# Performance work log

Measured on AMD Instinct MI355X. Metric: run time of the kernel, lower is better.

Reference implementation:

```python
import jax, jax.numpy as jnp
import numpy as np

EPS = 1e-5
GROUPS = 8

def group_norm(x, gamma, beta):
    b, c, h, w = x.shape
    xg = x.reshape(b, GROUPS, c // GROUPS, h, w)
    mean = xg.mean(axis=(2, 3, 4), keepdims=True)
    var = xg.var(axis=(2, 3, 4), keepdims=True)
    xn = ((xg - mean) * jax.lax.rsqrt(var + EPS)).reshape(b, c, h, w)
    return xn * gamma[None, :, None, None] + beta[None, :, None, None]

def conv1x1(x, w, b):
    # x: (B,C,H,W), w: (Cout,Cin), b: (Cout,)
    return jnp.einsum('bchw,oc->bohw', x, w) + b[None, :, None, None]

def setup_inputs() -> dict:
    key = jax.random.key(0)
    ks = jax.random.split(key, 10)
    C = 512
    x = jax.random.normal(ks[0], (4, C, 64, 64), dtype=jnp.float32)
    s = 1.0 / np.sqrt(C)
    inp = {
        'x': x,
        'gamma': jnp.ones((C,), jnp.float32),
        'beta': jnp.zeros((C,), jnp.float32),
        'wq': jax.random.uniform(ks[1], (C, C), jnp.float32, -s, s),
        'bq': jax.random.uniform(ks[2], (C,), jnp.float32, -s, s),
        'wk': jax.random.uniform(ks[3], (C, C), jnp.float32, -s, s),
        'bk': jax.random.uniform(ks[4], (C,), jnp.float32, -s, s),
        'wv': jax.random.uniform(ks[5], (C, C), jnp.float32, -s, s),
        'bv': jax.random.uniform(ks[6], (C,), jnp.float32, -s, s),
        'wo': jax.random.uniform(ks[7], (C, C), jnp.float32, -s, s),
        'bo': jax.random.uniform(ks[8], (C,), jnp.float32, -s, s),
    }
    return inp

def reference(x, gamma, beta, wq, bq, wk, bk, wv, bv, wo, bo):
    b, c, hd, wd = x.shape
    h = group_norm(x, gamma, beta)
    q = conv1x1(h, wq, bq).reshape(b, c, hd * wd).transpose(0, 2, 1)  # (b, hw, c)
    k = conv1x1(h, wk, bk).reshape(b, c, hd * wd)                      # (b, c, hw)
    v = conv1x1(h, wv, bv).reshape(b, c, hd * wd).transpose(0, 2, 1)  # (b, hw, c)
    attn = jnp.einsum('bqc,bck->bqk', q, k) * (c ** -0.5)
    attn = jax.nn.softmax(attn, axis=2)
    out = jnp.einsum('bqk,bkc->bqc', attn, v)                          # (b, hw, c)
    out = out.transpose(0, 2, 1).reshape(b, c, hd, wd)
    out = conv1x1(out, wo, bo)
    return x + out
```

## Files before the change

### kernel.cpp

```cpp
#include <hip/hip_runtime.h>
#include <stdint.h>

#define B_ 4
#define C_ 512
#define S_ 4096
#define G_ 8
#define CPG_ 64
#define EPS_ 1e-5f
#define SCALE_ 0.04419417382415922f
#define DTHR_ 4.0f

typedef _Float16 f16;
typedef _Float16 f16x8 __attribute__((ext_vector_type(8)));
typedef _Float16 f16x4 __attribute__((ext_vector_type(4)));
typedef unsigned short u16x8 __attribute__((ext_vector_type(8)));
typedef unsigned short u16x4 __attribute__((ext_vector_type(4)));
typedef unsigned int u32x4 __attribute__((ext_vector_type(4)));
typedef float f32x4 __attribute__((ext_vector_type(4)));

__device__ __forceinline__ float bf2f(unsigned short u) {
    union { unsigned int i; float f; } v; v.i = ((unsigned int)u) << 16; return v.f;
}
__device__ __forceinline__ unsigned short f2bf(float f) {
    union { float f; unsigned int i; } v; v.f = f;
    unsigned int i = v.i;
    return (unsigned short)((i + 0x7fffu + ((i >> 16) & 1u)) >> 16);
}
__device__ __forceinline__ unsigned char f2e4m3(float f) {
    return (unsigned char)(__builtin_amdgcn_cvt_pk_fp8_f32(f, f, 0, false) & 0xff);
}

__device__ __forceinline__ void bar_lgkm() {
    asm volatile("s_waitcnt lgkmcnt(0)" ::: "memory");
    __builtin_amdgcn_s_barrier();
}

#define DPPF(x, ctrl) __int_as_float(__builtin_amdgcn_update_dpp(0, __float_as_int(x), ctrl, 0xf, 0xf, true))
#define DPP_MAX16(x) do { \
    x = fmaxf(x, DPPF(x, 0x121)); \
    x = fmaxf(x, DPPF(x, 0x122)); \
    x = fmaxf(x, DPPF(x, 0x124)); \
    x = fmaxf(x, DPPF(x, 0x128)); \
} while (0)
#define DPP_SUM16(x) do { \
    x += DPPF(x, 0x121); \
    x += DPPF(x, 0x122); \
    x += DPPF(x, 0x124); \
    x += DPPF(x, 0x128); \
} while (0)

__global__ void detect_kernel(const void* __restrict__ gamma, int* __restrict__ flag, float* __restrict__ stats) {
    *flag = (((const unsigned int*)gamma)[0] != 0x3F800000u) ? 1 : 0;
    for (int i = 0; i < 64; ++i) stats[i] = 0.f;
}

__global__ __launch_bounds__(256) void cvt_weights(const void* __restrict__ w0, const void* __restrict__ w1,
                                                   const void* __restrict__ w2, const void* __restrict__ w3,
                                                   f16* __restrict__ dst, const int* __restrict__ flagp) {
    const void* srcs[4] = {w0, w1, w2, w3};
    const void* s = srcs[blockIdx.y];
    f16* d = dst + (size_t)blockIdx.y * (C_ * C_);
    int i4 = blockIdx.x * 256 + threadIdx.x;
    f16x4 o;
    if (*flagp) {
        u16x4 u = ((const u16x4*)s)[i4];
#pragma unroll
        for (int j = 0; j < 4; ++j) o[j] = (f16)bf2f(u[j]);
    } else {
        f32x4 u = ((const f32x4*)s)[i4];
#pragma unroll
        for (int j = 0; j < 4; ++j) o[j] = (f16)u[j];
    }
    ((f16x4*)d)[i4] = o;
}

__global__ __launch_bounds__(512) void cvt_vecs(const void* __restrict__ g, const void* __restrict__ be,
                                                const void* __restrict__ b1, const void* __restrict__ b2,
                                                const void* __restrict__ b3, const void* __restrict__ b4,
                                                float* __restrict__ dst, const int* __restrict__ flagp) {
    const void* srcs[6] = {g, be, b1, b2, b3, b4};
    const void* s = srcs[blockIdx.x];
    int i = threadIdx.x;
    dst[blockIdx.x * 512 + i] = (*flagp) ? bf2f(((const unsigned short*)s)[i]) : ((const float*)s)[i];
}

__global__ __launch_bounds__(1024) void gn_stats(const void* __restrict__ xraw, const int* __restrict__ flagp,
                                                 float* __restrict__ stats) {
    int bg = blockIdx.x >> 3, ch = blockIdx.x & 7;
    const int PER = CPG_ * S_ / 8;
    float s = 0.f, ss = 0.f;
    if (*flagp) {
        const u16x8* p = (const u16x8*)((const unsigned short*)xraw + (size_t)bg * CPG_ * S_ + (size_t)ch * PER);
        for (int i = threadIdx.x; i < PER / 8; i += 1024) {
            u16x8 u = p[i];
#pragma unroll
            for (int j = 0; j < 8; ++j) { float f = bf2f(u[j]); s += f; ss += f * f; }
        }
    } else {
        const f32x4* p = (const f32x4*)((const float*)xraw + (size_t)bg * CPG_ * S_ + (size_t)ch * PER);
        for (int i = threadIdx.x; i < PER / 4; i += 1024) {
            f32x4 u = p[i];
#pragma unroll
            for (int j = 0; j < 4; ++j) { float f = u[j]; s += f; ss += f * f; }
        }
    }
    __shared__ float rs[1024], rss[1024];
    rs[threadIdx.x] = s; rss[threadIdx.x] = ss;
    __syncthreads();
    for (int st = 512; st > 0; st >>= 1) {
        if (threadIdx.x < st) { rs[threadIdx.x] += rs[threadIdx.x + st]; rss[threadIdx.x] += rss[threadIdx.x + st]; }
        __syncthreads();
    }
    if (threadIdx.x == 0) {
        atomicAdd(&stats[bg * 2], rs[0]);
        atomicAdd(&stats[bg * 2 + 1], rss[0]);
    }
}

__global__ __launch_bounds__(256) void gn_apply_t(const void* __restrict__ xraw, const int* __restrict__ flagp,
                                                  const float* __restrict__ gammaF, const float* __restrict__ betaF,
                                                  const float* __restrict__ stats, f16* __restrict__ hT) {
    int s0 = blockIdx.x * 32, c0 = blockIdx.y * 32, b = blockIdx.z;
    __shared__ float tile[32][33];
    int t = threadIdx.x;
    int cr = t >> 3, ct = t & 7;
    int c = c0 + cr;
    int g = c >> 6;
    const float Ninv = 1.f / (float)(CPG_ * S_);
    float mean = stats[(b * G_ + g) * 2] * Ninv;
    float var = stats[(b * G_ + g) * 2 + 1] * Ninv - mean * mean;
    float rstd = rsqrtf(var + EPS_);
    float ga = gammaF[c], be = betaF[c];
    size_t xi = ((size_t)(b * C_ + c)) * S_ + s0;
    float v[4];
    if (*flagp) {
        u16x4 u = *(const u16x4*)((const unsigned short*)xraw + xi + ct * 4);
#pragma unroll
        for (int j = 0; j < 4; ++j) v[j] = bf2f(u[j]);
    } else {
        f32x4 u = *(const f32x4*)((const float*)xraw + xi + ct * 4);
#pragma unroll
        for (int j = 0; j < 4; ++j) v[j] = u[j];
    }
#pragma unroll
    for (int j = 0; j < 4; ++j)
        tile[cr][ct * 4 + j] = (v[j] - mean) * rstd * ga + be;
    __syncthreads();
    int sr = t >> 3, cv = t & 7;
    f16x4 o;
#pragma unroll
    for (int j = 0; j < 4; ++j) o[j] = (f16)tile[cv * 4 + j][sr];
    *(f16x4*)(hT + ((size_t)b * S_ + s0 + sr) * C_ + c0 + cv * 4) = o;
}

__global__ __launch_bounds__(256) void gemm_qk8(const f16* __restrict__ A, const f16* __restrict__ W,
                                                const float* __restrict__ biasF, unsigned char* __restrict__ out8) {
    int b = blockIdx.y;
    int s0 = (blockIdx.x >> 3) * 64;
    int o0 = (blockIdx.x & 7) * 64;
    __shared__ __attribute__((aligned(16))) f16 As[64][40];
    __shared__ __attribute__((aligned(16))) f16 Bs[64][40];
    int t = threadIdx.x;
    int w = t >> 6, lane = t & 63, l15 = lane & 15, quad = lane >> 4;
    f32x4 acc[4] = {};
    const f16* Ag = A + ((size_t)b * S_ + s0) * C_;
    int row = t >> 2, cp = (t & 3) * 8;
    const f16* aSrc = Ag + (size_t)row * C_ + cp;
    const f16* bSrc = W + (size_t)(o0 + row) * C_ + cp;
    f16x8 paA = *(const f16x8*)(aSrc);
    f16x8 pbA = *(const f16x8*)(bSrc);
    f16x8 paB = *(const f16x8*)(aSrc + 32);
    f16x8 pbB = *(const f16x8*)(bSrc + 32);
#pragma unroll
    for (int kk = 0; kk < 16; kk += 2) {
        *(f16x8*)(&As[row][cp]) = paA;
        *(f16x8*)(&Bs[row][cp]) = pbA;
        bar_lgkm();
        int ka = (kk * 32 + 64) & 511;
        paA = *(const f16x8*)(aSrc + ka);
        pbA = *(const f16x8*)(bSrc + ka);
        {
            f16x8 a = *(const f16x8*)&As[w * 16 + l15][quad * 8];
#pragma unroll
            for (int nt = 0; nt < 4; ++nt) {
                f16x8 bb = *(const f16x8*)&Bs[nt * 16 + l15][quad * 8];
                acc[nt] = __builtin_amdgcn_mfma_f32_16x16x32_f16(a, bb, acc[nt], 0, 0, 0);
            }
        }
        bar_lgkm();
        *(f16x8*)(&As[row][cp]) = paB;
        *(f16x8*)(&Bs[row][cp]) = pbB;
        bar_lgkm();
        int kb = (kk * 32 + 96) & 511;
        paB = *(const f16x8*)(aSrc + kb);
        pbB = *(const f16x8*)(bSrc + kb);
        {
            f16x8 a = *(const f16x8*)&As[w * 16 + l15][quad * 8];
#pragma unroll
            for (int nt = 0; nt < 4; ++nt) {
                f16x8 bb = *(const f16x8*)&Bs[nt * 16 + l15][quad * 8];
                acc[nt] = __builtin_amdgcn_mfma_f32_16x16x32_f16(a, bb, acc[nt], 0, 0, 0);
            }
        }
        bar_lgkm();
    }
#pragma unroll
    for (int nt = 0; nt < 4; ++nt) {
        int o = o0 + nt * 16 + l15;
        float bv = biasF[o];
#pragma unroll
        for (int r = 0; r < 4; ++r) {
            int s = s0 + w * 16 + quad * 4 + r;
            out8[((size_t)b * S_ + s) * C_ + o] = f2e4m3(acc[nt][r] + bv);
        }
    }
}

__global__ __launch_bounds__(256) void gemm_vt8(const f16* __restrict__ hT, const f16* __restrict__ W,
                                                const float* __restrict__ biasF, unsigned char* __restrict__ v8) {
    int b = blockIdx.y;
    int o0 = (blockIdx.x >> 6) * 64;
    int s0 = (blockIdx.x & 63) * 64;
    __shared__ __attribute__((aligned(16))) f16 As[64][40];
    __shared__ __attribute__((aligned(16))) f16 Bs[64][40];
    int t = threadIdx.x;
    int w = t >> 6, lane = t & 63, l15 = lane & 15, quad = lane >> 4;
    f32x4 acc[4] = {};
    const f16* Bg = hT + ((size_t)b * S_ + s0) * C_;
    int row = t >> 2, cp = (t & 3) * 8;
    const f16* aSrc = W + (size_t)(o0 + row) * C_ + cp;
    const f16* bSrc = Bg + (size_t)row * C_ + cp;
    f16x8 paA = *(const f16x8*)(aSrc);
    f16x8 pbA = *(const f16x8*)(bSrc);
    f16x8 paB = *(const f16x8*)(aSrc + 32);
    f16x8 pbB = *(const f16x8*)(bSrc + 32);
#pragma unroll
    for (int kk = 0; kk < 16; kk += 2) {
        *(f16x8*)(&As[row][cp]) = paA;
        *(f16x8*)(&Bs[row][cp]) = pbA;
        bar_lgkm();
        int ka = (kk * 32 + 64) & 511;
        paA = *(const f16x8*)(aSrc + ka);
        pbA = *(const f16x8*)(bSrc + ka);
        {
            f16x8 a = *(const f16x8*)&As[w * 16 + l15][quad * 8];
#pragma unroll
            for (int nt = 0; nt < 4; ++nt) {
                f16x8 bb = *(const f16x8*)&Bs[nt * 16 + l15][quad * 8];
                acc[nt] = __builtin_amdgcn_mfma_f32_16x16x32_f16(a, bb, acc[nt], 0, 0, 0);
            }
        }
        bar_lgkm();
        *(f16x8*)(&As[row][cp]) = paB;
        *(f16x8*)(&Bs[row][cp]) = pbB;
        bar_lgkm();
        int kb = (kk * 32 + 96) & 511;
        paB = *(const f16x8*)(aSrc + kb);
        pbB = *(const f16x8*)(bSrc + kb);
        {
            f16x8 a = *(const f16x8*)&As[w * 16 + l15][quad * 8];
#pragma unroll
            for (int nt = 0; nt < 4; ++nt) {
                f16x8 bb = *(const f16x8*)&Bs[nt * 16 + l15][quad * 8];
                acc[nt] = __builtin_amdgcn_mfma_f32_16x16x32_f16(a, bb, acc[nt], 0, 0, 0);
            }
        }
        bar_lgkm();
    }
    size_t tb = ((size_t)b * 64 + (s0 >> 6)) * 512;
#pragma unroll
    for (int nt = 0; nt < 4; ++nt) {
#pragma unroll
        for (int r = 0; r < 4; ++r) {
            int o = o0 + w * 16 + quad * 4 + r;
            v8[(tb + o) * 64 + nt * 16 + l15] = f2e4m3(acc[nt][r] + biasF[o]);
        }
    }
}

#define KST 136
#define VST 72
#define SLOT 9216
#define QST 528
#define RING_OFF 67584
#define PL_OFF   104448
#define REDM_OFF 113664
#define REDL_OFF 114688
#define SMEM_TOTAL 115712

__global__ __launch_bounds__(1024, 4) void flash_attn(const unsigned char* __restrict__ Q8,
                                                      const unsigned char* __restrict__ K8,
                                                      const unsigned char* __restrict__ V8,
                                                      f16* __restrict__ Op0, f16* __restrict__ Op1,
                                                      float* __restrict__ Ml, float* __restrict__ Ll) {
    extern __shared__ unsigned char smem[];
    unsigned char* Qlds = smem;
    unsigned char* ring = smem + RING_OFF;
    unsigned char* Pl   = smem + PL_OFF;
    float* redm = (float*)(smem + REDM_OFF);
    float* redl = (float*)(smem + REDL_OFF);

    const int id = blockIdx.x;
    const int b = (id & 7) >> 1;
    const int ks = id & 1;
    const int q0 = (id >> 3) * 128;
    const int kbase = ks * (S_ / 2);
    const int NT = (S_ / 2) / 64;

    const int t = threadIdx.x;
    const int w = t >> 6, lane = t & 63, l15 = lane & 15, quad = lane >> 4;
    const int qw = w >> 1;
    const int cw = w & 1;
    const int qrow = qw * 16 + l15;

    const unsigned char* Kb = K8 + (size_t)b * S_ * C_;
    const unsigned char* Vb = V8 + (size_t)b * 64 * 512 * 64;

    const int kwo = (((t & 15) >> 3) * SLOT) + ((t >> 4) * KST) + ((t & 7) * 16);
    const unsigned char* ksrc0 = Kb + (((size_t)(kbase + (t >> 4))) << 9) + ((t & 15) << 4);
    const int row16 = t >> 2;
    const int sel = (row16 >> 6) & 1;
    const int vr = (row16 & 63) + ((row16 >> 7) << 6);
    const int vwo = sel * SLOT + vr * VST + (t & 3) * 16;
    const int c0 = (row16 < 128) ? row16 : (128 + row16);
    const unsigned char* vsrc0 = Vb + (((size_t)(kbase >> 6)) << 15) + (c0 << 6) + ((t & 3) << 4);

    {
        const unsigned char* Qb = Q8 + ((size_t)b * S_ + q0) * C_;
        int qr = t >> 5, g16 = t & 31;
#pragma unroll
        for (int sg = 0; sg < 4; ++sg) {
            u32x4 v = *(const u32x4*)(Qb + (size_t)(sg * 32 + qr) * C_ + g16 * 16);
            *(u32x4*)&Qlds[(sg * 32 + qr) * QST + g16 * 16] = v;
        }
    }

    f32x4 accO[16] = {};
    float mrow[4], lrow[4];
#pragma unroll
    for (int r = 0; r < 4; ++r) { mrow[r] = -1e30f; lrow[r] = 0.f; }

    u32x4 pr0 = *(const u32x4*)(ksrc0);
    u32x4 pr1 = *(const u32x4*)(ksrc0 + 256);

    for (int tile = 0; tile < NT; ++tile) {
        const size_t toff = (size_t)tile << 15;
        const size_t tnoff = (size_t)((tile + 1) & 31) << 15;
        f32x4 accS[2] = {};

        {
            *(u32x4*)(ring + kwo) = pr0;
            pr0 = *(const u32x4*)(vsrc0 + toff);
            bar_lgkm();
            __builtin_amdgcn_s_setprio(1);
#pragma unroll
            for (int half = 0; half < 2; ++half) {
                const unsigned char* buf = &ring[half * SLOT];
#pragma unroll
                for (int cc2 = 0; cc2 < 4; ++cc2) {
                    long a = *(const long*)&Qlds[qrow * QST + (half * 4 + cc2) * 32 + quad * 8];
#pragma unroll
                    for (int nt = 0; nt < 2; ++nt) {
                        int row = cw * 32 + nt * 16 + l15;
                        long bb = *(const long*)&buf[row * KST + (cc2 * 4 + quad) * 8];
                        accS[nt] = __builtin_amdgcn_mfma_f32_16x16x32_fp8_fp8(a, bb, accS[nt], 0, 0, 0);
                    }
                }
            }
            __builtin_amdgcn_s_setprio(0);
        }
        {
            *(u32x4*)(ring + 2 * SLOT + kwo) = pr1;
            pr1 = *(const u32x4*)(vsrc0 + toff + 8192);
            bar_lgkm();
            __builtin_amdgcn_s_setprio(1);
#pragma unroll
            for (int half = 0; half < 2; ++half) {
                const unsigned char* buf = &ring[(2 + half) * SLOT];
#pragma unroll
                for (int cc2 = 0; cc2 < 4; ++cc2) {
                    long a = *(const long*)&Qlds[qrow * QST + ((2 + half) * 4 + cc2) * 32 + quad * 8];
#pragma unroll
                    for (int nt = 0; nt < 2; ++nt) {
                        int row = cw * 32 + nt * 16 + l15;
                        long bb = *(const long*)&buf[row * KST + (cc2 * 4 + quad) * 8];
                        accS[nt] = __builtin_amdgcn_mfma_f32_16x16x32_fp8_fp8(a, bb, accS[nt], 0, 0, 0);
                    }
                }
            }
            __builtin_amdgcn_s_setprio(0);
        }

        float sc[2][4];
#pragma unroll
        for (int nt = 0; nt < 2; ++nt)
#pragma unroll
            for (int r = 0; r < 4; ++r) sc[nt][r] = accS[nt][r] * SCALE_;

        float mx[4];
#pragma unroll
        for (int r = 0; r < 4; ++r) {
            mx[r] = fmaxf(sc[0][r], sc[1][r]);
            DPP_MAX16(mx[r]);
        }
        if (l15 == 0) {
#pragma unroll
            for (int r = 0; r < 4; ++r) redm[cw * 128 + qw * 16 + quad * 4 + r] = mx[r];
        }
        bar_lgkm();
        float alpha[4];
        int need = 0;
#pragma unroll
        for (int r = 0; r < 4; ++r) {
            int rowq = qw * 16 + quad * 4 + r;
            float mnew = fmaxf(mrow[r], fmaxf(redm[rowq], redm[128 + rowq]));
            if (mnew - mrow[r] > DTHR_) {
                alpha[r] = __expf(mrow[r] - mnew);
                mrow[r] = mnew;
                need = 1;
            } else {
                alpha[r] = 1.f;
            }
        }
        float p[2][4], psum[4];
#pragma unroll
        for (int r = 0; r < 4; ++r) {
            p[0][r] = __expf(sc[0][r] - mrow[r]);
            p[1][r] = __expf(sc[1][r] - mrow[r]);
            psum[r] = p[0][r] + p[1][r];
            DPP_SUM16(psum[r]);
        }
        if (l15 == 0) {
#pragma unroll
            for (int r = 0; r < 4; ++r) redl[cw * 128 + qw * 16 + quad * 4 + r] = psum[r];
        }
#pragma unroll
        for (int nt = 0; nt < 2; ++nt)
#pragma unroll
            for (int r = 0; r < 4; ++r)
                Pl[(qw * 16 + quad * 4 + r) * VST + cw * 32 + nt * 16 + l15] = f2e4m3(p[nt][r]);

        {
            *(u32x4*)(ring + vwo) = pr0;
            pr0 = *(const u32x4*)(ksrc0 + tnoff);
            bar_lgkm();
#pragma unroll
            for (int r = 0; r < 4; ++r) {
                int rowq = qw * 16 + quad * 4 + r;
                lrow[r] = lrow[r] * alpha[r] + redl[rowq] + redl[128 + rowq];
            }
            if (__any(need)) {
#pragma unroll
                for (int nt = 0; nt < 16; ++nt)
#pragma unroll
                    for (int r = 0; r < 4; ++r) accO[nt][r] *= alpha[r];
            }
            __builtin_amdgcn_s_setprio(1);
#pragma unroll
            for (int half = 0; half < 2; ++half) {
                const unsigned char* buf = &ring[half * SLOT];
#pragma unroll
                for (int st = 0; st < 2; ++st) {
                    long a = *(const long*)&Pl[(qw * 16 + l15) * VST + st * 32 + quad * 8];
#pragma unroll
                    for (int nt = 0; nt < 4; ++nt) {
                        int vrow = cw * 64 + nt * 16 + l15;
                        long bb = *(const long*)&buf[vrow * VST + (st * 4 + quad) * 8];
                        accO[half * 4 + nt] = __builtin_amdgcn_mfma_f32_16x16x32_fp8_fp8(a, bb, accO[half * 4 + nt], 0, 0, 0);
                    }
                }
            }
            __builtin_amdgcn_s_setprio(0);
        }
        {
            *(u32x4*)(ring + 2 * SLOT + vwo) = pr1;
            pr1 = *(const u32x4*)(ksrc0 + tnoff + 256);
            bar_lgkm();
            __builtin_amdgcn_s_setprio(1);
#pragma unroll
            for (int half = 0; half < 2; ++half) {
                const unsigned char* buf = &ring[(2 + half) * SLOT];
#pragma unroll
                for (int st = 0; st < 2; ++st) {
                    long a = *(const long*)&Pl[(qw * 16 + l15) * VST + st * 32 + quad * 8];
#pragma unroll
                    for (int nt = 0; nt < 4; ++nt) {
                        int vrow = cw * 64 + nt * 16 + l15;
                        long bb = *(const long*)&buf[vrow * VST + (st * 4 + quad) * 8];
                        accO[(2 + half) * 4 + nt] = __builtin_amdgcn_mfma_f32_16x16x32_fp8_fp8(a, bb, accO[(2 + half) * 4 + nt], 0, 0, 0);
                    }
                }
            }
            __builtin_amdgcn_s_setprio(0);
        }
    }

    __syncthreads();
    float li[4];
#pragma unroll
    for (int r = 0; r < 4; ++r) li[r] = 1.f / lrow[r];
    f16* Ob = (ks ? Op1 : Op0) + ((size_t)b * S_ + q0) * C_;
    f16* elds = (f16*)smem;
#pragma unroll
    for (int p = 0; p < 8; ++p) {
        if (qw == p) {
#pragma unroll
            for (int ntg = 0; ntg < 16; ++ntg) {
                int cc = cw * 256 + (ntg >> 2) * 64 + (ntg & 3) * 16 + l15;
#pragma unroll
                for (int r = 0; r < 4; ++r)
                    elds[(quad * 4 + r) * 520 + cc] = (f16)(accO[ntg][r] * li[r]);
            }
        }
        __syncthreads();
        {
            int erow = t >> 6, g8 = t & 63;
            f16x8 v = *(const f16x8*)&elds[erow * 520 + g8 * 8];
            *(f16x8*)(Ob + (size_t)(p * 16 + erow) * C_ + g8 * 8) = v;
        }
        __syncthreads();
    }
    if (cw == 0 && l15 == 0) {
        size_t base = (size_t)(b * 2 + ks) * S_ + q0 + qw * 16 + quad * 4;
#pragma unroll
        for (int r = 0; r < 4; ++r) { Ml[base + r] = mrow[r]; Ll[base + r] = lrow[r]; }
    }
}

__global__ __launch_bounds__(256) void merge_halves(const f16* __restrict__ Op0, const f16* __restrict__ Op1,
                                                    const float* __restrict__ Ml, const float* __restrict__ Ll,
                                                    f16* __restrict__ O) {
    int idx = blockIdx.x * 256 + threadIdx.x;
    int row = idx >> 6;
    int c8 = (idx & 63) * 8;
    int b = row >> 12, q = row & 4095;
    size_t i1 = (size_t)(b * 2) * S_ + q;
    size_t i2 = (size_t)(b * 2 + 1) * S_ + q;
    float m1 = Ml[i1], m2 = Ml[i2], l1 = Ll[i1], l2 = Ll[i2];
    float m = fmaxf(m1, m2);
    float u1 = __expf(m1 - m) * l1, u2 = __expf(m2 - m) * l2;
    float inv = 1.f / (u1 + u2);
    u1 *= inv; u2 *= inv;
    size_t ro = (size_t)(b * 4096 + q) * C_ + c8;
    f16x8 o1 = *(const f16x8*)(Op0 + ro);
    f16x8 o2 = *(const f16x8*)(Op1 + ro);
    f16x8 o;
#pragma unroll
    for (int j = 0; j < 8; ++j) o[j] = (f16)(u1 * (float)o1[j] + u2 * (float)o2[j]);
    *(f16x8*)(O + ro) = o;
}

__global__ __launch_bounds__(256) void gemm_out(const f16* __restrict__ A, const f16* __restrict__ W,
                                                const float* __restrict__ biasF,
                                                const void* __restrict__ xraw, const int* __restrict__ flagp,
                                                void* __restrict__ outraw) {
    int b = blockIdx.y;
    int s0 = (blockIdx.x >> 3) * 64;
    int o0 = (blockIdx.x & 7) * 64;
    __shared__ __attribute__((aligned(16))) f16 As[64][40];
    __shared__ __attribute__((aligned(16))) f16 Bs[64][40];
    int t = threadIdx.x;
    int w = t >> 6, lane = t & 63, l15 = lane & 15, quad = lane >> 4;
    f32x4 acc[4] = {};
    const f16* Ag = A + ((size_t)b * S_ + s0) * C_;
    int row = t >> 2, cp = (t & 3) * 8;
    const f16* aSrc = Ag + (size_t)row * C_ + cp;
    const f16* bSrc = W + (size_t)(o0 + row) * C_ + cp;
    f16x8 paA = *(const f16x8*)(aSrc);
    f16x8 pbA = *(const f16x8*)(bSrc);
    f16x8 paB = *(const f16x8*)(aSrc + 32);
    f16x8 pbB = *(const f16x8*)(bSrc + 32);
#pragma unroll
    for (int kk = 0; kk < 16; kk += 2) {
        *(f16x8*)(&As[row][cp]) = paA;
        *(f16x8*)(&Bs[row][cp]) = pbA;
        bar_lgkm();
        int ka = (kk * 32 + 64) & 511;
        paA = *(const f16x8*)(aSrc + ka);
        pbA = *(const f16x8*)(bSrc + ka);
        {
            f16x8 a = *(const f16x8*)&As[w * 16 + l15][quad * 8];
#pragma unroll
            for (int nt = 0; nt < 4; ++nt) {
                f16x8 bb = *(const f16x8*)&Bs[nt * 16 + l15][quad * 8];
                acc[nt] = __builtin_amdgcn_mfma_f32_16x16x32_f16(a, bb, acc[nt], 0, 0, 0);
            }
        }
        bar_lgkm();
        *(f16x8*)(&As[row][cp]) = paB;
        *(f16x8*)(&Bs[row][cp]) = pbB;
        bar_lgkm();
        int kb = (kk * 32 + 96) & 511;
        paB = *(const f16x8*)(aSrc + kb);
        pbB = *(const f16x8*)(bSrc + kb);
        {
            f16x8 a = *(const f16x8*)&As[w * 16 + l15][quad * 8];
#pragma unroll
            for (int nt = 0; nt < 4; ++nt) {
                f16x8 bb = *(const f16x8*)&Bs[nt * 16 + l15][quad * 8];
                acc[nt] = __builtin_amdgcn_mfma_f32_16x16x32_f16(a, bb, acc[nt], 0, 0, 0);
            }
        }
        bar_lgkm();
    }
    int flg = *flagp;
#pragma unroll
    for (int nt = 0; nt < 4; ++nt) {
        int o = o0 + nt * 16 + l15;
        float bv = biasF[o];
        int sbase = s0 + w * 16 + quad * 4;
        size_t xi = ((size_t)b * C_ + o) * S_ + sbase;
        if (flg) {
            u16x4 xr = *(const u16x4*)((const unsigned short*)xraw + xi);
            u16x4 res;
#pragma unroll
            for (int r = 0; r < 4; ++r) res[r] = f2bf(acc[nt][r] + bv + bf2f(xr[r]));
            *(u16x4*)((unsigned short*)outraw + xi) = res;
        } else {
            f32x4 xr = *(const f32x4*)((const float*)xraw + xi);
            f32x4 res;
#pragma unroll
            for (int r = 0; r < 4; ++r) res[r] = acc[nt][r] + bv + xr[r];
            *(f32x4*)((float*)outraw + xi) = res;
        }
    }
}

extern "C" void kernel_launch(void* const* d_in, const int* in_sizes, int n_in,
                              void* d_out, int out_size, void* d_ws, size_t ws_size,
                              hipStream_t stream) {
    const void* x     = d_in[0];
    const void* gamma = d_in[1];
    const void* beta  = d_in[2];
    const void* wq    = d_in[3];
    const void* bq    = d_in[4];
    const void* wk    = d_in[5];
    const void* bk    = d_in[6];
    const void* wv    = d_in[7];
    const void* bv    = d_in[8];
    const void* wo    = d_in[9];
    const void* bo    = d_in[10];

    char* ws = (char*)d_ws;
    size_t off = 0;
    int* flag = (int*)(ws + off); off += 256;
    float* stats = (float*)(ws + off); off += 512;
    float* vecF = (float*)(ws + off); off += 6 * 512 * 4;
    float* Ml = (float*)(ws + off); off += (size_t)2 * B_ * S_ * 4;
    float* Ll = (float*)(ws + off); off += (size_t)2 * B_ * S_ * 4;
    f16* w16 = (f16*)(ws + off); off += (size_t)4 * C_ * C_ * 2;
    const size_t TEN = (size_t)B_ * S_ * C_ * 2;
    const size_t TE8 = (size_t)B_ * S_ * C_;
    f16* hT  = (f16*)(ws + off); off += TEN;
    unsigned char* q8 = (unsigned char*)(ws + off); off += TE8;
    unsigned char* k8 = (unsigned char*)(ws + off); off += TE8;
    unsigned char* v8 = (unsigned char*)(ws + off); off += TE8;
    f16* o_  = (f16*)(ws + off); off += TEN;
    f16* op1 = (f16*)(ws + off); off += TEN;
    if (ws_size < off) return;

    float* gammaF = vecF + 0 * 512;
    float* betaF  = vecF + 1 * 512;
    float* bqF    = vecF + 2 * 512;
    float* bkF    = vecF + 3 * 512;
    float* bvF    = vecF + 4 * 512;
    float* boF    = vecF + 5 * 512;
    f16* wq16 = w16 + 0 * (size_t)C_ * C_;
    f16* wk16 = w16 + 1 * (size_t)C_ * C_;
    f16* wv16 = w16 + 2 * (size_t)C_ * C_;
    f16* wo16 = w16 + 3 * (size_t)C_ * C_;

    hipFuncSetAttribute((const void*)flash_attn, hipFuncAttributeMaxDynamicSharedMemorySize, SMEM_TOTAL);

    detect_kernel<<<dim3(1), dim3(1), 0, stream>>>(gamma, flag, stats);
    cvt_weights<<<dim3(256, 4), dim3(256), 0, stream>>>(wq, wk, wv, wo, w16, flag);
    cvt_vecs<<<dim3(6), dim3(512), 0, stream>>>(gamma, beta, bq, bk, bv, bo, vecF, flag);
    gn_stats<<<dim3(256), dim3(1024), 0, stream>>>(x, flag, stats);
    gn_apply_t<<<dim3(128, 16, 4), dim3(256), 0, stream>>>(x, flag, gammaF, betaF, stats, hT);
    gemm_qk8<<<dim3(512, 4), dim3(256), 0, stream>>>(hT, wq16, bqF, q8);
    gemm_qk8<<<dim3(512, 4), dim3(256), 0, stream>>>(hT, wk16, bkF, k8);
    gemm_vt8<<<dim3(512, 4), dim3(256), 0, stream>>>(hT, wv16, bvF, v8);
    flash_attn<<<dim3(256), dim3(1024), SMEM_TOTAL, stream>>>(q8, k8, v8, hT, op1, Ml, Ll);
    merge_halves<<<dim3((B_ * S_ * C_ / 8) / 256), dim3(256), 0, stream>>>(hT, op1, Ml, Ll, o_);
    gemm_out<<<dim3(512, 4), dim3(256), 0, stream>>>(o_, wo16, boF, x, flag, d_out);
}
```

Before: 409.4 us.

## Halve flash-attn query tile to 64 rows, fold softmax scale into Q

The flash attention kernel now uses 512-thread blocks covering 64 query rows instead of 1024 threads covering 128, with twice as many blocks and a smaller LDS footprint. The K/V prefetch is redone so each thread loads two 16-byte chunks per stage. The softmax scale and log2(e) are folded into the Q projection before FP8 quantization, and the exponentials switch to native exp2. The rescale threshold rises to 5.5. Smaller tiles raise occupancy but double K/V reloads per query. Pre-scaling Q changes the FP8 quantization range, and the higher threshold lets partial sums grow larger before rescaling.

```diff
diff --git a/kernel.cpp b/kernel.cpp
--- a/kernel.cpp
+++ b/kernel.cpp
@@ -8,7 +8,8 @@
 #define CPG_ 64
 #define EPS_ 1e-5f
 #define SCALE_ 0.04419417382415922f
-#define DTHR_ 4.0f
+#define LOG2E_ 1.4426950408889634f
+#define DTHR_ 5.5f
 
 typedef _Float16 f16;
 typedef _Float16 f16x8 __attribute__((ext_vector_type(8)));
@@ -28,6 +29,9 @@
 }
 __device__ __forceinline__ unsigned char f2e4m3(float f) {
     return (unsigned char)(__builtin_amdgcn_cvt_pk_fp8_f32(f, f, 0, false) & 0xff);
+}
+__device__ __forceinline__ float fast_exp2(float x) {
+    return __builtin_amdgcn_exp2f(x);
 }
 
 __device__ __forceinline__ void bar_lgkm() {
@@ -154,7 +158,8 @@
 }
 
 __global__ __launch_bounds__(256) void gemm_qk8(const f16* __restrict__ A, const f16* __restrict__ W,
-                                                const float* __restrict__ biasF, unsigned char* __restrict__ out8) {
+                                                const float* __restrict__ biasF, unsigned char* __restrict__ out8,
+                                                float ascale) {
     int b = blockIdx.y;
     int s0 = (blockIdx.x >> 3) * 64;
     int o0 = (blockIdx.x & 7) * 64;
@@ -211,7 +216,7 @@
 #pragma unroll
         for (int r = 0; r < 4; ++r) {
             int s = s0 + w * 16 + quad * 4 + r;
-            out8[((size_t)b * S_ + s) * C_ + o] = f2e4m3(acc[nt][r] + bv);
+            out8[((size_t)b * S_ + s) * C_ + o] = f2e4m3((acc[nt][r] + bv) * ascale);
         }
     }
 }
@@ -282,28 +287,28 @@
 #define VST 72
 #define SLOT 9216
 #define QST 528
-#define RING_OFF 67584
-#define PL_OFF   104448
-#define REDM_OFF 113664
-#define REDL_OFF 114688
-#define SMEM_TOTAL 115712
-
-__global__ __launch_bounds__(1024, 4) void flash_attn(const unsigned char* __restrict__ Q8,
-                                                      const unsigned char* __restrict__ K8,
-                                                      const unsigned char* __restrict__ V8,
-                                                      f16* __restrict__ Op0, f16* __restrict__ Op1,
-                                                      float* __restrict__ Ml, float* __restrict__ Ll) {
+#define PL_OFF   36864
+#define REDM_OFF 41472
+#define REDL_OFF 41984
+#define Q_OFF    42496
+#define SMEM_TOTAL 76288
+
+__global__ __launch_bounds__(512, 4) void flash_attn(const unsigned char* __restrict__ Q8,
+                                                     const unsigned char* __restrict__ K8,
+                                                     const unsigned char* __restrict__ V8,
+                                                     f16* __restrict__ Op0, f16* __restrict__ Op1,
+                                                     float* __restrict__ Ml, float* __restrict__ Ll) {
     extern __shared__ unsigned char smem[];
-    unsigned char* Qlds = smem;
-    unsigned char* ring = smem + RING_OFF;
+    unsigned char* ring = smem;
     unsigned char* Pl   = smem + PL_OFF;
     float* redm = (float*)(smem + REDM_OFF);
     float* redl = (float*)(smem + REDL_OFF);
+    unsigned char* Qlds = smem + Q_OFF;
 
     const int id = blockIdx.x;
     const int b = (id & 7) >> 1;
     const int ks = id & 1;
-    const int q0 = (id >> 3) * 128;
+    const int q0 = (id >> 3) * 64;
     const int kbase = ks * (S_ / 2);
     const int NT = (S_ / 2) / 64;
 
@@ -317,21 +322,22 @@
     const unsigned char* Vb = V8 + (size_t)b * 64 * 512 * 64;
 
     const int kwo = (((t & 15) >> 3) * SLOT) + ((t >> 4) * KST) + ((t & 7) * 16);
-    const unsigned char* ksrc0 = Kb + (((size_t)(kbase + (t >> 4))) << 9) + ((t & 15) << 4);
+    const unsigned char* ksrc = Kb + (((size_t)(kbase + (t >> 4))) << 9) + ((t & 15) << 4);
     const int row16 = t >> 2;
-    const int sel = (row16 >> 6) & 1;
-    const int vr = (row16 & 63) + ((row16 >> 7) << 6);
-    const int vwo = sel * SLOT + vr * VST + (t & 3) * 16;
-    const int c0 = (row16 < 128) ? row16 : (128 + row16);
-    const unsigned char* vsrc0 = Vb + (((size_t)(kbase >> 6)) << 15) + (c0 << 6) + ((t & 3) << 4);
+    const int vwo = ((row16 >> 6) & 1) * SLOT + (row16 & 63) * VST + (t & 3) * 16;
+    const unsigned char* vsrc = Vb + (((size_t)(kbase >> 6)) << 15) + (row16 << 6) + ((t & 3) << 4);
+
+    u32x4 prA = *(const u32x4*)(ksrc);
+    u32x4 prB = *(const u32x4*)(ksrc + 16384);
 
     {
         const unsigned char* Qb = Q8 + ((size_t)b * S_ + q0) * C_;
         int qr = t >> 5, g16 = t & 31;
 #pragma unroll
-        for (int sg = 0; sg < 4; ++sg) {
-            u32x4 v = *(const u32x4*)(Qb + (size_t)(sg * 32 + qr) * C_ + g16 * 16);
-            *(u32x4*)&Qlds[(sg * 32 + qr) * QST + g16 * 16] = v;
+        for (int j = 0; j < 4; ++j) {
+            int row = j * 16 + qr;
+            u32x4 v = *(const u32x4*)(Qb + (size_t)row * C_ + g16 * 16);
+            *(u32x4*)&Qlds[row * QST + g16 * 16] = v;
         }
     }
 
@@ -339,9 +345,6 @@
     float mrow[4], lrow[4];
 #pragma unroll
     for (int r = 0; r < 4; ++r) { mrow[r] = -1e30f; lrow[r] = 0.f; }
-
-    u32x4 pr0 = *(const u32x4*)(ksrc0);
-    u32x4 pr1 = *(const u32x4*)(ksrc0 + 256);
 
     for (int tile = 0; tile < NT; ++tile) {
         const size_t toff = (size_t)tile << 15;
@@ -349,8 +352,10 @@
         f32x4 accS[2] = {};
 
         {
-            *(u32x4*)(ring + kwo) = pr0;
-            pr0 = *(const u32x4*)(vsrc0 + toff);
+            *(u32x4*)(ring + kwo) = prA;
+            *(u32x4*)(ring + kwo + 32 * KST) = prB;
+            prA = *(const u32x4*)(ksrc + toff + 256);
+            prB = *(const u32x4*)(ksrc + toff + 256 + 16384);
             bar_lgkm();
             __builtin_amdgcn_s_setprio(1);
 #pragma unroll
@@ -370,8 +375,10 @@
             __builtin_amdgcn_s_setprio(0);
         }
         {
-            *(u32x4*)(ring + 2 * SLOT + kwo) = pr1;
-            pr1 = *(const u32x4*)(vsrc0 + toff + 8192);
+            *(u32x4*)(ring + 2 * SLOT + kwo) = prA;
+            *(u32x4*)(ring + 2 * SLOT + kwo + 32 * KST) = prB;
+            prA = *(const u32x4*)(vsrc + toff);
+            prB = *(const u32x4*)(vsrc + toff + 16384);
             bar_lgkm();
             __builtin_amdgcn_s_setprio(1);
 #pragma unroll
@@ -391,21 +398,15 @@
             __builtin_amdgcn_s_setprio(0);
         }
 
-        float sc[2][4];
-#pragma unroll
-        for (int nt = 0; nt < 2; ++nt)
-#pragma unroll
-            for (int r = 0; r < 4; ++r) sc[nt][r] = accS[nt][r] * SCALE_;
-
         float mx[4];
 #pragma unroll
         for (int r = 0; r < 4; ++r) {
-            mx[r] = fmaxf(sc[0][r], sc[1][r]);
+            mx[r] = fmaxf(accS[0][r], accS[1][r]);
             DPP_MAX16(mx[r]);
         }
         if (l15 == 0) {
 #pragma unroll
-            for (int r = 0; r < 4; ++r) redm[cw * 128 + qw * 16 + quad * 4 + r] = mx[r];
+            for (int r = 0; r < 4; ++r) redm[cw * 64 + qw * 16 + quad * 4 + r] = mx[r];
         }
         bar_lgkm();
         float alpha[4];
@@ -413,9 +414,9 @@
 #pragma unroll
         for (int r = 0; r < 4; ++r) {
             int rowq = qw * 16 + quad * 4 + r;
-            float mnew = fmaxf(mrow[r], fmaxf(redm[rowq], redm[128 + rowq]));
+            float mnew = fmaxf(mrow[r], fmaxf(redm[rowq], redm[64 + rowq]));
             if (mnew - mrow[r] > DTHR_) {
-                alpha[r] = __expf(mrow[r] - mnew);
+                alpha[r] = fast_exp2(mrow[r] - mnew);
                 mrow[r] = mnew;
                 need = 1;
             } else {
@@ -425,14 +426,14 @@
         float p[2][4], psum[4];
 #pragma unroll
         for (int r = 0; r < 4; ++r) {
-            p[0][r] = __expf(sc[0][r] - mrow[r]);
-            p[1][r] = __expf(sc[1][r] - mrow[r]);
+            p[0][r] = fast_exp2(accS[0][r] - mrow[r]);
+            p[1][r] = fast_exp2(accS[1][r] - mrow[r]);
             psum[r] = p[0][r] + p[1][r];
             DPP_SUM16(psum[r]);
         }
         if (l15 == 0) {
 #pragma unroll
-            for (int r = 0; r < 4; ++r) redl[cw * 128 + qw * 16 + quad * 4 + r] = psum[r];
+            for (int r = 0; r < 4; ++r) redl[cw * 64 + qw * 16 + quad * 4 + r] = psum[r];
         }
 #pragma unroll
         for (int nt = 0; nt < 2; ++nt)
@@ -441,13 +442,15 @@
                 Pl[(qw * 16 + quad * 4 + r) * VST + cw * 32 + nt * 16 + l15] = f2e4m3(p[nt][r]);
 
         {
-            *(u32x4*)(ring + vwo) = pr0;
-            pr0 = *(const u32x4*)(ksrc0 + tnoff);
+            *(u32x4*)(ring + vwo) = prA;
+            *(u32x4*)(ring + vwo + 64 * VST) = prB;
+            prA = *(const u32x4*)(vsrc + toff + 8192);
+            prB = *(const u32x4*)(vsrc + toff + 8192 + 16384);
             bar_lgkm();
 #pragma unroll
             for (int r = 0; r < 4; ++r) {
                 int rowq = qw * 16 + quad * 4 + r;
-                lrow[r] = lrow[r] * alpha[r] + redl[rowq] + redl[128 + rowq];
+                lrow[r] = lrow[r] * alpha[r] + redl[rowq] + redl[64 + rowq];
             }
             if (__any(need)) {
 #pragma unroll
@@ -473,8 +476,10 @@
             __builtin_amdgcn_s_setprio(0);
         }
         {
-            *(u32x4*)(ring + 2 * SLOT + vwo) = pr1;
-            pr1 = *(const u32x4*)(ksrc0 + tnoff + 256);
+            *(u32x4*)(ring + 2 * SLOT + vwo) = prA;
+            *(u32x4*)(ring + 2 * SLOT + vwo + 64 * VST) = prB;
+            prA = *(const u32x4*)(ksrc + tnoff);
+            prB = *(const u32x4*)(ksrc + tnoff + 16384);
             bar_lgkm();
             __builtin_amdgcn_s_setprio(1);
 #pragma unroll
@@ -502,7 +507,7 @@
     f16* Ob = (ks ? Op1 : Op0) + ((size_t)b * S_ + q0) * C_;
     f16* elds = (f16*)smem;
 #pragma unroll
-    for (int p = 0; p < 8; ++p) {
+    for (int p = 0; p < 4; ++p) {
         if (qw == p) {
 #pragma unroll
             for (int ntg = 0; ntg < 16; ++ntg) {
@@ -513,8 +518,10 @@
             }
         }
         __syncthreads();
-        {
-            int erow = t >> 6, g8 = t & 63;
+#pragma unroll
+        for (int e = 0; e < 2; ++e) {
+            int erow = (t >> 6) + e * 8;
+            int g8 = t & 63;
             f16x8 v = *(const f16x8*)&elds[erow * 520 + g8 * 8];
             *(f16x8*)(Ob + (size_t)(p * 16 + erow) * C_ + g8 * 8) = v;
         }
@@ -538,7 +545,7 @@
     size_t i2 = (size_t)(b * 2 + 1) * S_ + q;
     float m1 = Ml[i1], m2 = Ml[i2], l1 = Ll[i1], l2 = Ll[i2];
     float m = fmaxf(m1, m2);
-    float u1 = __expf(m1 - m) * l1, u2 = __expf(m2 - m) * l2;
+    float u1 = fast_exp2(m1 - m) * l1, u2 = fast_exp2(m2 - m) * l2;
     float inv = 1.f / (u1 + u2);
     u1 *= inv; u2 *= inv;
     size_t ro = (size_t)(b * 4096 + q) * C_ + c8;
@@ -670,17 +677,17 @@
     f16* wv16 = w16 + 2 * (size_t)C_ * C_;
     f16* wo16 = w16 + 3 * (size_t)C_ * C_;
 
-    hipFuncSetAttribute((const void*)flash_attn, hipFuncAttributeMaxDynamicSharedMemorySize, SMEM_TOTAL);
+    (void)hipFuncSetAttribute((const void*)flash_attn, hipFuncAttributeMaxDynamicSharedMemorySize, SMEM_TOTAL);
 
     detect_kernel<<<dim3(1), dim3(1), 0, stream>>>(gamma, flag, stats);
     cvt_weights<<<dim3(256, 4), dim3(256), 0, stream>>>(wq, wk, wv, wo, w16, flag);
     cvt_vecs<<<dim3(6), dim3(512), 0, stream>>>(gamma, beta, bq, bk, bv, bo, vecF, flag);
     gn_stats<<<dim3(256), dim3(1024), 0, stream>>>(x, flag, stats);
     gn_apply_t<<<dim3(128, 16, 4), dim3(256), 0, stream>>>(x, flag, gammaF, betaF, stats, hT);
-    gemm_qk8<<<dim3(512, 4), dim3(256), 0, stream>>>(hT, wq16, bqF, q8);
-    gemm_qk8<<<dim3(512, 4), dim3(256), 0, stream>>>(hT, wk16, bkF, k8);
+    gemm_qk8<<<dim3(512, 4), dim3(256), 0, stream>>>(hT, wq16, bqF, q8, SCALE_ * LOG2E_);
+    gemm_qk8<<<dim3(512, 4), dim3(256), 0, stream>>>(hT, wk16, bkF, k8, 1.0f);
     gemm_vt8<<<dim3(512, 4), dim3(256), 0, stream>>>(hT, wv16, bvF, v8);
-    flash_attn<<<dim3(256), dim3(1024), SMEM_TOTAL, stream>>>(q8, k8, v8, hT, op1, Ml, Ll);
+    flash_attn<<<dim3(512), dim3(512), SMEM_TOTAL, stream>>>(q8, k8, v8, hT, op1, Ml, Ll);
     merge_halves<<<dim3((B_ * S_ * C_ / 8) / 256), dim3(256), 0, stream>>>(hT, op1, Ml, Ll, o_);
     gemm_out<<<dim3(512, 4), dim3(256), 0, stream>>>(o_, wo16, boF, x, flag, d_out);
 }
```

Result: slower. 444.1 us (+8.5%).

## Use 128x128 GEMM tiles and fold softmax scale and log2e into Q

Applied to the files above, without the earlier changes.

Replaces the three 64x64-tile projection GEMMs with a shared 128x128-tile core in which each wave computes a 4x4 block of MFMA tiles. This raises data reuse per shared-memory load and cuts block count. The softmax scale times log2(e) is folded into the Q projection before fp8 quantisation, so the attention kernel drops its per-score multiply and uses hardware exp2. The rescale threshold is also raised. Scaling Q before the fp8 cast changes quantisation error, and a larger threshold allows larger unnormalised exponents.

```diff
diff --git a/kernel.cpp b/kernel.cpp
--- a/kernel.cpp
+++ b/kernel.cpp
@@ -8,7 +8,8 @@
 #define CPG_ 64
 #define EPS_ 1e-5f
 #define SCALE_ 0.04419417382415922f
-#define DTHR_ 4.0f
+#define LOG2E_ 1.4426950408889634f
+#define DTHR_ 5.5f
 
 typedef _Float16 f16;
 typedef _Float16 f16x8 __attribute__((ext_vector_type(8)));
@@ -28,6 +29,9 @@
 }
 __device__ __forceinline__ unsigned char f2e4m3(float f) {
     return (unsigned char)(__builtin_amdgcn_cvt_pk_fp8_f32(f, f, 0, false) & 0xff);
+}
+__device__ __forceinline__ float fast_exp2(float x) {
+    return __builtin_amdgcn_exp2f(x);
 }
 
 __device__ __forceinline__ void bar_lgkm() {
@@ -153,127 +157,117 @@
     *(f16x4*)(hT + ((size_t)b * S_ + s0 + sr) * C_ + c0 + cv * 4) = o;
 }
 
+#define GEMM128_CORE(Aptr, Bptr)                                                             \
+    __shared__ __attribute__((aligned(16))) f16 As[128][40];                                  \
+    __shared__ __attribute__((aligned(16))) f16 Bs[128][40];                                  \
+    int t = threadIdx.x;                                                                      \
+    int w = t >> 6, lane = t & 63, l15 = lane & 15, quad = lane >> 4;                         \
+    int wr = w >> 1, wc = w & 1;                                                              \
+    f32x4 acc[4][4] = {};                                                                     \
+    int srow = t >> 1, scol = (t & 1) * 8;                                                    \
+    const f16* aS = (Aptr) + (size_t)srow * C_ + scol;                                        \
+    const f16* bS = (Bptr) + (size_t)srow * C_ + scol;                                        \
+    f16x8 pa0 = *(const f16x8*)(aS);                                                          \
+    f16x8 pa1 = *(const f16x8*)(aS + 16);                                                     \
+    f16x8 pb0 = *(const f16x8*)(bS);                                                          \
+    f16x8 pb1 = *(const f16x8*)(bS + 16);                                                     \
+    _Pragma("unroll")                                                                         \
+    for (int kk = 0; kk < 16; ++kk) {                                                         \
+        *(f16x8*)(&As[srow][scol]) = pa0;                                                     \
+        *(f16x8*)(&As[srow][scol + 16]) = pa1;                                                \
+        *(f16x8*)(&Bs[srow][scol]) = pb0;                                                     \
+        *(f16x8*)(&Bs[srow][scol + 16]) = pb1;                                                \
+        int kn = ((kk + 1) & 15) * 32;                                                        \
+        pa0 = *(const f16x8*)(aS + kn);                                                       \
+        pa1 = *(const f16x8*)(aS + kn + 16);                                                  \
+        pb0 = *(const f16x8*)(bS + kn);                                                       \
+        pb1 = *(const f16x8*)(bS + kn + 16);                                                  \
+        bar_lgkm();                                                                           \
+        f16x8 af[4], bf[4];                                                                   \
+        _Pragma("unroll")                                                                     \
+        for (int i = 0; i < 4; ++i) {                                                         \
+            af[i] = *(const f16x8*)&As[wr * 64 + i * 16 + l15][quad * 8];                     \
+            bf[i] = *(const f16x8*)&Bs[wc * 64 + i * 16 + l15][quad * 8];                     \
+        }                                                                                     \
+        _Pragma("unroll")                                                                     \
+        for (int mi = 0; mi < 4; ++mi)                                                        \
+            _Pragma("unroll")                                                                 \
+            for (int ni = 0; ni < 4; ++ni)                                                    \
+                acc[mi][ni] = __builtin_amdgcn_mfma_f32_16x16x32_f16(af[mi], bf[ni], acc[mi][ni], 0, 0, 0); \
+        bar_lgkm();                                                                           \
+    }
+
 __global__ __launch_bounds__(256) void gemm_qk8(const f16* __restrict__ A, const f16* __restrict__ W,
-                                                const float* __restrict__ biasF, unsigned char* __restrict__ out8) {
-    int b = blockIdx.y;
-    int s0 = (blockIdx.x >> 3) * 64;
-    int o0 = (blockIdx.x & 7) * 64;
-    __shared__ __attribute__((aligned(16))) f16 As[64][40];
-    __shared__ __attribute__((aligned(16))) f16 Bs[64][40];
-    int t = threadIdx.x;
-    int w = t >> 6, lane = t & 63, l15 = lane & 15, quad = lane >> 4;
-    f32x4 acc[4] = {};
-    const f16* Ag = A + ((size_t)b * S_ + s0) * C_;
-    int row = t >> 2, cp = (t & 3) * 8;
-    const f16* aSrc = Ag + (size_t)row * C_ + cp;
-    const f16* bSrc = W + (size_t)(o0 + row) * C_ + cp;
-    f16x8 paA = *(const f16x8*)(aSrc);
-    f16x8 pbA = *(const f16x8*)(bSrc);
-    f16x8 paB = *(const f16x8*)(aSrc + 32);
-    f16x8 pbB = *(const f16x8*)(bSrc + 32);
-#pragma unroll
-    for (int kk = 0; kk < 16; kk += 2) {
-        *(f16x8*)(&As[row][cp]) = paA;
-        *(f16x8*)(&Bs[row][cp]) = pbA;
-        bar_lgkm();
-        int ka = (kk * 32 + 64) & 511;
-        paA = *(const f16x8*)(aSrc + ka);
-        pbA = *(const f16x8*)(bSrc + ka);
-        {
-            f16x8 a = *(const f16x8*)&As[w * 16 + l15][quad * 8];
-#pragma unroll
-            for (int nt = 0; nt < 4; ++nt) {
-                f16x8 bb = *(const f16x8*)&Bs[nt * 16 + l15][quad * 8];
-                acc[nt] = __builtin_amdgcn_mfma_f32_16x16x32_f16(a, bb, acc[nt], 0, 0, 0);
-            }
-        }
-        bar_lgkm();
-        *(f16x8*)(&As[row][cp]) = paB;
-        *(f16x8*)(&Bs[row][cp]) = pbB;
-        bar_lgkm();
-        int kb = (kk * 32 + 96) & 511;
-        paB = *(const f16x8*)(aSrc + kb);
-        pbB = *(const f16x8*)(bSrc + kb);
-        {
-            f16x8 a = *(const f16x8*)&As[w * 16 + l15][quad * 8];
-#pragma unroll
-            for (int nt = 0; nt < 4; ++nt) {
-                f16x8 bb = *(const f16x8*)&Bs[nt * 16 + l15][quad * 8];
-                acc[nt] = __builtin_amdgcn_mfma_f32_16x16x32_f16(a, bb, acc[nt], 0, 0, 0);
-            }
-        }
-        bar_lgkm();
-    }
-#pragma unroll
-    for (int nt = 0; nt < 4; ++nt) {
-        int o = o0 + nt * 16 + l15;
-        float bv = biasF[o];
-#pragma unroll
-        for (int r = 0; r < 4; ++r) {
-            int s = s0 + w * 16 + quad * 4 + r;
-            out8[((size_t)b * S_ + s) * C_ + o] = f2e4m3(acc[nt][r] + bv);
+                                                const float* __restrict__ biasF, unsigned char* __restrict__ out8,
+                                                float ascale) {
+    int m0 = (blockIdx.x >> 2) * 128;
+    int n0 = (blockIdx.x & 3) * 128;
+    GEMM128_CORE(A + (size_t)m0 * C_, W + (size_t)n0 * C_)
+#pragma unroll
+    for (int ni = 0; ni < 4; ++ni) {
+        int n = n0 + wc * 64 + ni * 16 + l15;
+        float bv = biasF[n];
+#pragma unroll
+        for (int mi = 0; mi < 4; ++mi) {
+            int mb = m0 + wr * 64 + mi * 16 + quad * 4;
+#pragma unroll
+            for (int r = 0; r < 4; ++r)
+                out8[(size_t)(mb + r) * C_ + n] = f2e4m3((acc[mi][ni][r] + bv) * ascale);
         }
     }
 }
 
 __global__ __launch_bounds__(256) void gemm_vt8(const f16* __restrict__ hT, const f16* __restrict__ W,
                                                 const float* __restrict__ biasF, unsigned char* __restrict__ v8) {
-    int b = blockIdx.y;
-    int o0 = (blockIdx.x >> 6) * 64;
-    int s0 = (blockIdx.x & 63) * 64;
-    __shared__ __attribute__((aligned(16))) f16 As[64][40];
-    __shared__ __attribute__((aligned(16))) f16 Bs[64][40];
-    int t = threadIdx.x;
-    int w = t >> 6, lane = t & 63, l15 = lane & 15, quad = lane >> 4;
-    f32x4 acc[4] = {};
-    const f16* Bg = hT + ((size_t)b * S_ + s0) * C_;
-    int row = t >> 2, cp = (t & 3) * 8;
-    const f16* aSrc = W + (size_t)(o0 + row) * C_ + cp;
-    const f16* bSrc = Bg + (size_t)row * C_ + cp;
-    f16x8 paA = *(const f16x8*)(aSrc);
-    f16x8 pbA = *(const f16x8*)(bSrc);
-    f16x8 paB = *(const f16x8*)(aSrc + 32);
-    f16x8 pbB = *(const f16x8*)(bSrc + 32);
-#pragma unroll
-    for (int kk = 0; kk < 16; kk += 2) {
-        *(f16x8*)(&As[row][cp]) = paA;
-        *(f16x8*)(&Bs[row][cp]) = pbA;
-        bar_lgkm();
-        int ka = (kk * 32 + 64) & 511;
-        paA = *(const f16x8*)(aSrc + ka);
-        pbA = *(const f16x8*)(bSrc + ka);
-        {
-            f16x8 a = *(const f16x8*)&As[w * 16 + l15][quad * 8];
-#pragma unroll
-            for (int nt = 0; nt < 4; ++nt) {
-                f16x8 bb = *(const f16x8*)&Bs[nt * 16 + l15][quad * 8];
-                acc[nt] = __builtin_amdgcn_mfma_f32_16x16x32_f16(a, bb, acc[nt], 0, 0, 0);
-            }
-        }
-        bar_lgkm();
-        *(f16x8*)(&As[row][cp]) = paB;
-        *(f16x8*)(&Bs[row][cp]) = pbB;
-        bar_lgkm();
-        int kb = (kk * 32 + 96) & 511;
-        paB = *(const f16x8*)(aSrc + kb);
-        pbB = *(const f16x8*)(bSrc + kb);
-        {
-            f16x8 a = *(const f16x8*)&As[w * 16 + l15][quad * 8];
-#pragma unroll
-            for (int nt = 0; nt < 4; ++nt) {
-                f16x8 bb = *(const f16x8*)&Bs[nt * 16 + l15][quad * 8];
-                acc[nt] = __builtin_amdgcn_mfma_f32_16x16x32_f16(a, bb, acc[nt], 0, 0, 0);
-            }
-        }
-        bar_lgkm();
-    }
-    size_t tb = ((size_t)b * 64 + (s0 >> 6)) * 512;
-#pragma unroll
-    for (int nt = 0; nt < 4; ++nt) {
-#pragma unroll
-        for (int r = 0; r < 4; ++r) {
-            int o = o0 + w * 16 + quad * 4 + r;
-            v8[(tb + o) * 64 + nt * 16 + l15] = f2e4m3(acc[nt][r] + biasF[o]);
+    int m0 = (blockIdx.x & 3) * 128;
+    int n0 = (blockIdx.x >> 2) * 128;
+    GEMM128_CORE(W + (size_t)m0 * C_, hT + (size_t)n0 * C_)
+#pragma unroll
+    for (int ni = 0; ni < 4; ++ni) {
+        int gn = n0 + wc * 64 + ni * 16 + l15;
+        int bb = gn >> 12, s = gn & 4095;
+        size_t tb = ((size_t)(bb * 64 + (s >> 6)) * 512);
+        int sc = s & 63;
+#pragma unroll
+        for (int mi = 0; mi < 4; ++mi) {
+            int ob = m0 + wr * 64 + mi * 16 + quad * 4;
+#pragma unroll
+            for (int r = 0; r < 4; ++r)
+                v8[(tb + ob + r) * 64 + sc] = f2e4m3(acc[mi][ni][r] + biasF[ob + r]);
+        }
+    }
+}
+
+__global__ __launch_bounds__(256) void gemm_out(const f16* __restrict__ A, const f16* __restrict__ W,
+                                                const float* __restrict__ biasF,
+                                                const void* __restrict__ xraw, const int* __restrict__ flagp,
+                                                void* __restrict__ outraw) {
+    int m0 = (blockIdx.x >> 2) * 128;
+    int n0 = (blockIdx.x & 3) * 128;
+    GEMM128_CORE(A + (size_t)m0 * C_, W + (size_t)n0 * C_)
+    int flg = *flagp;
+#pragma unroll
+    for (int ni = 0; ni < 4; ++ni) {
+        int o = n0 + wc * 64 + ni * 16 + l15;
+        float bv = biasF[o];
+#pragma unroll
+        for (int mi = 0; mi < 4; ++mi) {
+            int gm = m0 + wr * 64 + mi * 16 + quad * 4;
+            int bb = gm >> 12, s = gm & 4095;
+            size_t xi = ((size_t)(bb * C_ + o)) * S_ + s;
+            if (flg) {
+                u16x4 xr = *(const u16x4*)((const unsigned short*)xraw + xi);
+                u16x4 res;
+#pragma unroll
+                for (int r = 0; r < 4; ++r) res[r] = f2bf(acc[mi][ni][r] + bv + bf2f(xr[r]));
+                *(u16x4*)((unsigned short*)outraw + xi) = res;
+            } else {
+                f32x4 xr = *(const f32x4*)((const float*)xraw + xi);
+                f32x4 res;
+#pragma unroll
+                for (int r = 0; r < 4; ++r) res[r] = acc[mi][ni][r] + bv + xr[r];
+                *(f32x4*)((float*)outraw + xi) = res;
+            }
         }
     }
 }
@@ -391,16 +385,10 @@
             __builtin_amdgcn_s_setprio(0);
         }
 
-        float sc[2][4];
-#pragma unroll
-        for (int nt = 0; nt < 2; ++nt)
-#pragma unroll
-            for (int r = 0; r < 4; ++r) sc[nt][r] = accS[nt][r] * SCALE_;
-
         float mx[4];
 #pragma unroll
         for (int r = 0; r < 4; ++r) {
-            mx[r] = fmaxf(sc[0][r], sc[1][r]);
+            mx[r] = fmaxf(accS[0][r], accS[1][r]);
             DPP_MAX16(mx[r]);
         }
         if (l15 == 0) {
@@ -415,7 +403,7 @@
             int rowq = qw * 16 + quad * 4 + r;
             float mnew = fmaxf(mrow[r], fmaxf(redm[rowq], redm[128 + rowq]));
             if (mnew - mrow[r] > DTHR_) {
-                alpha[r] = __expf(mrow[r] - mnew);
+                alpha[r] = fast_exp2(mrow[r] - mnew);
                 mrow[r] = mnew;
                 need = 1;
             } else {
@@ -425,8 +413,8 @@
         float p[2][4], psum[4];
 #pragma unroll
         for (int r = 0; r < 4; ++r) {
-            p[0][r] = __expf(sc[0][r] - mrow[r]);
-            p[1][r] = __expf(sc[1][r] - mrow[r]);
+            p[0][r] = fast_exp2(accS[0][r] - mrow[r]);
+            p[1][r] = fast_exp2(accS[1][r] - mrow[r]);
             psum[r] = p[0][r] + p[1][r];
             DPP_SUM16(psum[r]);
         }
@@ -538,7 +526,7 @@
     size_t i2 = (size_t)(b * 2 + 1) * S_ + q;
     float m1 = Ml[i1], m2 = Ml[i2], l1 = Ll[i1], l2 = Ll[i2];
     float m = fmaxf(m1, m2);
-    float u1 = __expf(m1 - m) * l1, u2 = __expf(m2 - m) * l2;
+    float u1 = fast_exp2(m1 - m) * l1, u2 = fast_exp2(m2 - m) * l2;
     float inv = 1.f / (u1 + u2);
     u1 *= inv; u2 *= inv;
     size_t ro = (size_t)(b * 4096 + q) * C_ + c8;
@@ -548,82 +536,6 @@
 #pragma unroll
     for (int j = 0; j < 8; ++j) o[j] = (f16)(u1 * (float)o1[j] + u2 * (float)o2[j]);
     *(f16x8*)(O + ro) = o;
-}
-
-__global__ __launch_bounds__(256) void gemm_out(const f16* __restrict__ A, const f16* __restrict__ W,
-                                                const float* __restrict__ biasF,
-                                                const void* __restrict__ xraw, const int* __restrict__ flagp,
-                                                void* __restrict__ outraw) {
-    int b = blockIdx.y;
-    int s0 = (blockIdx.x >> 3) * 64;
-    int o0 = (blockIdx.x & 7) * 64;
-    __shared__ __attribute__((aligned(16))) f16 As[64][40];
-    __shared__ __attribute__((aligned(16))) f16 Bs[64][40];
-    int t = threadIdx.x;
-    int w = t >> 6, lane = t & 63, l15 = lane & 15, quad = lane >> 4;
-    f32x4 acc[4] = {};
-    const f16* Ag = A + ((size_t)b * S_ + s0) * C_;
-    int row = t >> 2, cp = (t & 3) * 8;
-    const f16* aSrc = Ag + (size_t)row * C_ + cp;
-    const f16* bSrc = W + (size_t)(o0 + row) * C_ + cp;
-    f16x8 paA = *(const f16x8*)(aSrc);
-    f16x8 pbA = *(const f16x8*)(bSrc);
-    f16x8 paB = *(const f16x8*)(aSrc + 32);
-    f16x8 pbB = *(const f16x8*)(bSrc + 32);
-#pragma unroll
-    for (int kk = 0; kk < 16; kk += 2) {
-        *(f16x8*)(&As[row][cp]) = paA;
-        *(f16x8*)(&Bs[row][cp]) = pbA;
-        bar_lgkm();
-        int ka = (kk * 32 + 64) & 511;
-        paA = *(const f16x8*)(aSrc + ka);
-        pbA = *(const f16x8*)(bSrc + ka);
-        {
-            f16x8 a = *(const f16x8*)&As[w * 16 + l15][quad * 8];
-#pragma unroll
-            for (int nt = 0; nt < 4; ++nt) {
-                f16x8 bb = *(const f16x8*)&Bs[nt * 16 + l15][quad * 8];
-                acc[nt] = __builtin_amdgcn_mfma_f32_16x16x32_f16(a, bb, acc[nt], 0, 0, 0);
-            }
-        }
-        bar_lgkm();
-        *(f16x8*)(&As[row][cp]) = paB;
-        *(f16x8*)(&Bs[row][cp]) = pbB;
-        bar_lgkm();
-        int kb = (kk * 32 + 96) & 511;
-        paB = *(const f16x8*)(aSrc + kb);
-        pbB = *(const f16x8*)(bSrc + kb);
-        {
-            f16x8 a = *(const f16x8*)&As[w * 16 + l15][quad * 8];
-#pragma unroll
-            for (int nt = 0; nt < 4; ++nt) {
-                f16x8 bb = *(const f16x8*)&Bs[nt * 16 + l15][quad * 8];
-                acc[nt] = __builtin_amdgcn_mfma_f32_16x16x32_f16(a, bb, acc[nt], 0, 0, 0);
-            }
-        }
-        bar_lgkm();
-    }
-    int flg = *flagp;
-#pragma unroll
-    for (int nt = 0; nt < 4; ++nt) {
-        int o = o0 + nt * 16 + l15;
-        float bv = biasF[o];
-        int sbase = s0 + w * 16 + quad * 4;
-        size_t xi = ((size_t)b * C_ + o) * S_ + sbase;
-        if (flg) {
-            u16x4 xr = *(const u16x4*)((const unsigned short*)xraw + xi);
-            u16x4 res;
-#pragma unroll
-            for (int r = 0; r < 4; ++r) res[r] = f2bf(acc[nt][r] + bv + bf2f(xr[r]));
-            *(u16x4*)((unsigned short*)outraw + xi) = res;
-        } else {
-            f32x4 xr = *(const f32x4*)((const float*)xraw + xi);
-            f32x4 res;
-#pragma unroll
-            for (int r = 0; r < 4; ++r) res[r] = acc[nt][r] + bv + xr[r];
-            *(f32x4*)((float*)outraw + xi) = res;
-        }
-    }
 }
 
 extern "C" void kernel_launch(void* const* d_in, const int* in_sizes, int n_in,
@@ -670,17 +582,17 @@
     f16* wv16 = w16 + 2 * (size_t)C_ * C_;
     f16* wo16 = w16 + 3 * (size_t)C_ * C_;
 
-    hipFuncSetAttribute((const void*)flash_attn, hipFuncAttributeMaxDynamicSharedMemorySize, SMEM_TOTAL);
+    (void)hipFuncSetAttribute((const void*)flash_attn, hipFuncAttributeMaxDynamicSharedMemorySize, SMEM_TOTAL);
 
     detect_kernel<<<dim3(1), dim3(1), 0, stream>>>(gamma, flag, stats);
     cvt_weights<<<dim3(256, 4), dim3(256), 0, stream>>>(wq, wk, wv, wo, w16, flag);
     cvt_vecs<<<dim3(6), dim3(512), 0, stream>>>(gamma, beta, bq, bk, bv, bo, vecF, flag);
     gn_stats<<<dim3(256), dim3(1024), 0, stream>>>(x, flag, stats);
     gn_apply_t<<<dim3(128, 16, 4), dim3(256), 0, stream>>>(x, flag, gammaF, betaF, stats, hT);
-    gemm_qk8<<<dim3(512, 4), dim3(256), 0, stream>>>(hT, wq16, bqF, q8);
-    gemm_qk8<<<dim3(512, 4), dim3(256), 0, stream>>>(hT, wk16, bkF, k8);
-    gemm_vt8<<<dim3(512, 4), dim3(256), 0, stream>>>(hT, wv16, bvF, v8);
+    gemm_qk8<<<dim3(512), dim3(256), 0, stream>>>(hT, wq16, bqF, q8, SCALE_ * LOG2E_);
+    gemm_qk8<<<dim3(512), dim3(256), 0, stream>>>(hT, wk16, bkF, k8, 1.0f);
+    gemm_vt8<<<dim3(512), dim3(256), 0, stream>>>(hT, wv16, bvF, v8);
     flash_attn<<<dim3(256), dim3(1024), SMEM_TOTAL, stream>>>(q8, k8, v8, hT, op1, Ml, Ll);
     merge_halves<<<dim3((B_ * S_ * C_ / 8) / 256), dim3(256), 0, stream>>>(hT, op1, Ml, Ll, o_);
-    gemm_out<<<dim3(512, 4), dim3(256), 0, stream>>>(o_, wo16, boF, x, flag, d_out);
-}
+    gemm_out<<<dim3(512), dim3(256), 0, stream>>>(o_, wo16, boF, x, flag, d_out);
+}
```

Measured after the change: 383.9 us. -6.2%, faster.
